# Kernel tuning notes

Hardware: AMD Instinct MI355X
Metric: run time of the kernel (lower is better)

Reference implementation:

```python
import jax, jax.numpy as jnp
import numpy as np

B, I, O = 512, 1024, 1024

def setup_inputs() -> dict:
    key = jax.random.key(0)
    kx, kw = jax.random.split(key)
    x = jax.random.normal(kx, (B, I), dtype=jnp.float32)
    W = jax.random.normal(kw, (O, I), dtype=jnp.float32)
    return {"x": x, "W": W}

def reference(x, W):
    # Tropical (max-plus) linear map: y[b, o] = max_i (x[b, i] + W[o, i])
    # Faithful to the torch broadcast-add + max-reduce formulation.
    out = x[..., None, :] + W[None, :, :]  # [B, O, I]
    return jnp.max(out, axis=-1)           # [B, O]
```

## Files before the change

kernel.cpp:

```cpp
#include <hip/hip_runtime.h>
#include <float.h>


#define B_DIM 512
#define I_DIM 1024
#define O_DIM 1024
#define BT 128
#define OT 128
#define KT 8

__device__ __forceinline__ void g2lds16(const float* g, float* l) {
    __builtin_amdgcn_global_load_lds(
        (const __attribute__((address_space(1))) void*)g,
        (__attribute__((address_space(3))) void*)l, 16, 0, 0);
}

__device__ __forceinline__ unsigned pack2h(float a, float b) {
    const unsigned lo = (unsigned)__builtin_bit_cast(unsigned short, (_Float16)a);
    const unsigned hi = (unsigned)__builtin_bit_cast(unsigned short, (_Float16)b);
    return lo | (hi << 16);
}
__device__ __forceinline__ float lo16f(unsigned u) {
    return (float)__builtin_bit_cast(_Float16, (unsigned short)(u & 0xffffu));
}
__device__ __forceinline__ float hi16f(unsigned u) {
    return (float)__builtin_bit_cast(_Float16, (unsigned short)(u >> 16));
}

template <int KB>
__global__ __launch_bounds__(256, 2) void trop_main(
    const float* __restrict__ xT,
    const float* __restrict__ wT,
    _Float16* __restrict__ part)
{
    constexpr int NCH = KB / KT;
    static_assert(KB % KT == 0, "");
    __shared__ __align__(16) float xs[4][2][KT * 32];
    __shared__ __align__(16) float ws[4][2][KT * 128];

    const int tid  = threadIdx.x;
    const int wave = tid >> 6;
    const int lane = tid & 63;
    const int to   = lane & 15;
    const int tbw  = lane >> 4;
    const int o0 = blockIdx.x * OT;
    const int b0 = blockIdx.y * BT;
    const int bw0 = b0 + 32 * wave;
    const int kz = blockIdx.z;
    const int kbase = kz * KB;

    const int rk8 = lane >> 3;
    const int xc4 = (lane & 7) * 4;
    const int rk2 = lane >> 5;
    const int wc4 = (lane & 31) * 4;

    float acc[8][8];
    #pragma unroll
    for (int i = 0; i < 8; ++i)
        #pragma unroll
        for (int j = 0; j < 8; ++j)
            acc[i][j] = -FLT_MAX;

    auto stage = [&](int c, int buf) {
        const int k0 = kbase + c * KT;
        g2lds16(&xT[(size_t)(k0 + rk8) * B_DIM + bw0 + xc4],
                &xs[wave][buf][0]);
        #pragma unroll
        for (int t = 0; t < 4; ++t)
            g2lds16(&wT[(size_t)(k0 + 2 * t + rk2) * O_DIM + o0 + wc4],
                    &ws[wave][buf][t * 256]);
    };

    auto compute = [&](int buf) {
        const float* xB = &xs[wave][buf][4 * tbw];
        const float* wB = &ws[wave][buf][4 * to];
        #pragma unroll
        for (int k = 0; k < KT; k += 2) {
            const float4 xa0 = *(const float4*)&xB[k * 32];
            const float4 xa1 = *(const float4*)&xB[k * 32 + 16];
            const float4 xb0 = *(const float4*)&xB[(k + 1) * 32];
            const float4 xb1 = *(const float4*)&xB[(k + 1) * 32 + 16];
            const float4 wa0 = *(const float4*)&wB[k * 128];
            const float4 wa1 = *(const float4*)&wB[k * 128 + 64];
            const float4 wb0 = *(const float4*)&wB[(k + 1) * 128];
            const float4 wb1 = *(const float4*)&wB[(k + 1) * 128 + 64];

            const float xa[8] = {xa0.x, xa0.y, xa0.z, xa0.w, xa1.x, xa1.y, xa1.z, xa1.w};
            const float xb[8] = {xb0.x, xb0.y, xb0.z, xb0.w, xb1.x, xb1.y, xb1.z, xb1.w};
            const float wa[8] = {wa0.x, wa0.y, wa0.z, wa0.w, wa1.x, wa1.y, wa1.z, wa1.w};
            const float wb[8] = {wb0.x, wb0.y, wb0.z, wb0.w, wb1.x, wb1.y, wb1.z, wb1.w};

            #pragma unroll
            for (int i = 0; i < 8; ++i)
                #pragma unroll
                for (int j = 0; j < 8; ++j) {
                    const float s0 = xa[i] + wa[j];
                    const float s1 = xb[i] + wb[j];
                    acc[i][j] = fmaxf(acc[i][j], fmaxf(s0, s1));
                }
        }
    };

    stage(0, 0);
    #pragma unroll
    for (int c = 0; c < NCH; ++c) {
        if (c + 1 < NCH) stage(c + 1, (c + 1) & 1);
        compute(c & 1);
    }

    _Float16* pout = part + (size_t)kz * (B_DIM * O_DIM);
    #pragma unroll
    for (int i = 0; i < 8; ++i) {
        const int b = bw0 + (i >> 2) * 16 + 4 * tbw + (i & 3);
        const uint2 v0 = make_uint2(pack2h(acc[i][0], acc[i][1]),
                                    pack2h(acc[i][2], acc[i][3]));
        const uint2 v1 = make_uint2(pack2h(acc[i][4], acc[i][5]),
                                    pack2h(acc[i][6], acc[i][7]));
        *(uint2*)((char*)pout + ((size_t)b * O_DIM + o0 + 4 * to) * 2)      = v0;
        *(uint2*)((char*)pout + ((size_t)b * O_DIM + o0 + 64 + 4 * to) * 2) = v1;
    }
}

__global__ __launch_bounds__(256) void transpose3(
    const float* __restrict__ x, float* __restrict__ xT,
    const float* __restrict__ W, float* __restrict__ wT)
{
    __shared__ float tile[32][33];
    const int tx = threadIdx.x;
    const int ty = threadIdx.y;
    const int z  = blockIdx.z;
    const float* in; float* out; int dst_ld;
    if (z == 0) { in = x;                  out = xT;            dst_ld = B_DIM; }
    else        { in = W + (size_t)(z - 1) * 512 * I_DIM;
                  out = wT + (z - 1) * 512;                     dst_ld = O_DIM; }
    const int r0 = blockIdx.y * 32;
    const int c0 = blockIdx.x * 32;
    #pragma unroll
    for (int i = 0; i < 4; ++i)
        tile[ty + 8 * i][tx] = in[(size_t)(r0 + ty + 8 * i) * I_DIM + c0 + tx];
    __syncthreads();
    #pragma unroll
    for (int i = 0; i < 4; ++i)
        out[(size_t)(c0 + ty + 8 * i) * dst_ld + r0 + tx] = tile[tx][ty + 8 * i];
}

template <int KS>
__global__ __launch_bounds__(256) void trop_reduce_h(
    const _Float16* __restrict__ part, float* __restrict__ y)
{
    constexpr size_t N = (size_t)B_DIM * O_DIM;
    const int idx = blockIdx.x * 256 + threadIdx.x;
    float m0 = -FLT_MAX, m1 = -FLT_MAX, m2 = -FLT_MAX, m3 = -FLT_MAX;
    float m4 = -FLT_MAX, m5 = -FLT_MAX, m6 = -FLT_MAX, m7 = -FLT_MAX;
    #pragma unroll
    for (int s = 0; s < KS; ++s) {
        const uint4 v = *(const uint4*)((const char*)part + (s * N + (size_t)idx * 8) * 2);
        m0 = fmaxf(m0, lo16f(v.x)); m1 = fmaxf(m1, hi16f(v.x));
        m2 = fmaxf(m2, lo16f(v.y)); m3 = fmaxf(m3, hi16f(v.y));
        m4 = fmaxf(m4, lo16f(v.z)); m5 = fmaxf(m5, hi16f(v.z));
        m6 = fmaxf(m6, lo16f(v.w)); m7 = fmaxf(m7, hi16f(v.w));
    }
    const float4 o0 = make_float4(m0, m1, m2, m3);
    const float4 o1 = make_float4(m4, m5, m6, m7);
    ((float4*)y)[2 * idx]     = o0;
    ((float4*)y)[2 * idx + 1] = o1;
}

__global__ __launch_bounds__(256) void trop_naive(
    const float* __restrict__ x, const float* __restrict__ W,
    float* __restrict__ y)
{
    const int idx = blockIdx.x * 256 + threadIdx.x;
    const int b = idx / O_DIM, o = idx % O_DIM;
    float m = -FLT_MAX;
    for (int i = 0; i < I_DIM; ++i)
        m = fmaxf(m, x[b * I_DIM + i] + W[o * I_DIM + i]);
    y[idx] = m;
}

extern "C" void kernel_launch(void* const* d_in, const int* in_sizes, int n_in,
                              void* d_out, int out_size, void* d_ws, size_t ws_size,
                              hipStream_t stream) {
    const float* x = (const float*)d_in[0];
    const float* W = (const float*)d_in[1];
    float* y = (float*)d_out;

    const size_t slab_h = (size_t)B_DIM * O_DIM * 2;
    const size_t xT_sz  = (size_t)B_DIM * I_DIM * sizeof(float);
    const size_t wT_sz  = (size_t)O_DIM * I_DIM * sizeof(float);
    const dim3 rgrid(B_DIM * O_DIM / 8 / 256);
    const dim3 tgrid(I_DIM / 32, 512 / 32, 3);
    const dim3 tblk(32, 8);

    if (ws_size >= 16 * slab_h + xT_sz + wT_sz) {
        _Float16* part = (_Float16*)d_ws;
        float* xT = (float*)((char*)d_ws + 16 * slab_h);
        float* wT = xT + (size_t)B_DIM * I_DIM;
        transpose3<<<tgrid, tblk, 0, stream>>>(x, xT, W, wT);
        trop_main<I_DIM / 16><<<dim3(O_DIM / OT, B_DIM / BT, 16), 256, 0, stream>>>(xT, wT, part);
        trop_reduce_h<16><<<rgrid, 256, 0, stream>>>(part, y);
    } else if (ws_size >= 8 * slab_h + xT_sz + wT_sz) {
        _Float16* part = (_Float16*)d_ws;
        float* xT = (float*)((char*)d_ws + 8 * slab_h);
        float* wT = xT + (size_t)B_DIM * I_DIM;
        transpose3<<<tgrid, tblk, 0, stream>>>(x, xT, W, wT);
        trop_main<I_DIM / 8><<<dim3(O_DIM / OT, B_DIM / BT, 8), 256, 0, stream>>>(xT, wT, part);
        trop_reduce_h<8><<<rgrid, 256, 0, stream>>>(part, y);
    } else if (ws_size >= slab_h + xT_sz + wT_sz) {
        _Float16* part = (_Float16*)d_ws;
        float* xT = (float*)((char*)d_ws + slab_h);
        float* wT = xT + (size_t)B_DIM * I_DIM;
        transpose3<<<tgrid, tblk, 0, stream>>>(x, xT, W, wT);
        trop_main<I_DIM><<<dim3(O_DIM / OT, B_DIM / BT, 1), 256, 0, stream>>>(xT, wT, part);
        trop_reduce_h<1><<<rgrid, 256, 0, stream>>>(part, y);
    } else {
        trop_naive<<<dim3(B_DIM * O_DIM / 256), 256, 0, stream>>>(x, W, y);
    }
}
```

Before: 86.94 us.

## Compute tropical max-plus in packed fp16 with v_pk_add/v_pk_max

Converts x and W to fp16 in the prep kernel: x keeps its row layout and W is transposed. The main kernel then runs the add and max on packed half2 values through inline v_pk_add_f16 and v_pk_max_f16, which halves the VALU instruction count per element pair. LDS staging and global loads move half as many bytes, and the x tile layout changes so each lane reads contiguous k values along with a new output store pattern. The cost is that the additions are now done in fp16 rather than fp32, which adds rounding error beyond the existing fp16 partial storage.

```diff
diff --git a/kernel.cpp b/kernel.cpp
--- a/kernel.cpp
+++ b/kernel.cpp
@@ -5,21 +5,32 @@
 #define B_DIM 512
 #define I_DIM 1024
 #define O_DIM 1024
-#define BT 128
-#define OT 128
-#define KT 8
-
-__device__ __forceinline__ void g2lds16(const float* g, float* l) {
+#define KT 16
+
+__device__ __forceinline__ void g2lds16(const void* g, void* l) {
     __builtin_amdgcn_global_load_lds(
         (const __attribute__((address_space(1))) void*)g,
         (__attribute__((address_space(3))) void*)l, 16, 0, 0);
 }
 
-__device__ __forceinline__ unsigned pack2h(float a, float b) {
-    const unsigned lo = (unsigned)__builtin_bit_cast(unsigned short, (_Float16)a);
-    const unsigned hi = (unsigned)__builtin_bit_cast(unsigned short, (_Float16)b);
-    return lo | (hi << 16);
-}
+__device__ __forceinline__ unsigned pk_add_bl(unsigned w, unsigned x) {
+    unsigned d;
+    asm("v_pk_add_f16 %0, %1, %2 op_sel:[0,0] op_sel_hi:[1,0]"
+        : "=v"(d) : "v"(w), "v"(x));
+    return d;
+}
+__device__ __forceinline__ unsigned pk_add_bh(unsigned w, unsigned x) {
+    unsigned d;
+    asm("v_pk_add_f16 %0, %1, %2 op_sel:[0,1] op_sel_hi:[1,1]"
+        : "=v"(d) : "v"(w), "v"(x));
+    return d;
+}
+__device__ __forceinline__ unsigned pk_max(unsigned a, unsigned b) {
+    unsigned d;
+    asm("v_pk_max_f16 %0, %1, %2" : "=v"(d) : "v"(a), "v"(b));
+    return d;
+}
+
 __device__ __forceinline__ float lo16f(unsigned u) {
     return (float)__builtin_bit_cast(_Float16, (unsigned short)(u & 0xffffu));
 }
@@ -29,75 +40,77 @@
 
 template <int KB>
 __global__ __launch_bounds__(256, 2) void trop_main(
-    const float* __restrict__ xT,
-    const float* __restrict__ wT,
+    const _Float16* __restrict__ xh,
+    const _Float16* __restrict__ wh,
     _Float16* __restrict__ part)
 {
     constexpr int NCH = KB / KT;
     static_assert(KB % KT == 0, "");
-    __shared__ __align__(16) float xs[4][2][KT * 32];
-    __shared__ __align__(16) float ws[4][2][KT * 128];
+    __shared__ __align__(16) char xs[4][2][32 * KT * 2];
+    __shared__ __align__(16) char ws[4][2][KT * 128 * 2];
 
     const int tid  = threadIdx.x;
     const int wave = tid >> 6;
     const int lane = tid & 63;
     const int to   = lane & 15;
     const int tbw  = lane >> 4;
-    const int o0 = blockIdx.x * OT;
-    const int b0 = blockIdx.y * BT;
-    const int bw0 = b0 + 32 * wave;
-    const int kz = blockIdx.z;
+    const int o0  = blockIdx.x * 128;
+    const int bw0 = blockIdx.y * 128 + 32 * wave;
+    const int kz  = blockIdx.z;
     const int kbase = kz * KB;
 
-    const int rk8 = lane >> 3;
-    const int xc4 = (lane & 7) * 4;
-    const int rk2 = lane >> 5;
-    const int wc4 = (lane & 31) * 4;
-
-    float acc[8][8];
+    const int xb_l = lane >> 1;
+    const int xk_l = (lane & 1) * 16;
+    const int wk_l = lane >> 4;
+    const int wc_l = (lane & 15) * 16;
+
+    unsigned acc_u[8][4];
     #pragma unroll
     for (int i = 0; i < 8; ++i)
         #pragma unroll
-        for (int j = 0; j < 8; ++j)
-            acc[i][j] = -FLT_MAX;
+        for (int p = 0; p < 4; ++p)
+            acc_u[i][p] = 0xFC00FC00u;
 
     auto stage = [&](int c, int buf) {
         const int k0 = kbase + c * KT;
-        g2lds16(&xT[(size_t)(k0 + rk8) * B_DIM + bw0 + xc4],
+        g2lds16((const char*)xh + ((size_t)(bw0 + xb_l) * I_DIM + k0) * 2 + xk_l,
                 &xs[wave][buf][0]);
         #pragma unroll
         for (int t = 0; t < 4; ++t)
-            g2lds16(&wT[(size_t)(k0 + 2 * t + rk2) * O_DIM + o0 + wc4],
-                    &ws[wave][buf][t * 256]);
+            g2lds16((const char*)wh + ((size_t)(k0 + 4 * t + wk_l) * O_DIM + o0) * 2 + wc_l,
+                    &ws[wave][buf][t * 1024]);
     };
 
     auto compute = [&](int buf) {
-        const float* xB = &xs[wave][buf][4 * tbw];
-        const float* wB = &ws[wave][buf][4 * to];
-        #pragma unroll
-        for (int k = 0; k < KT; k += 2) {
-            const float4 xa0 = *(const float4*)&xB[k * 32];
-            const float4 xa1 = *(const float4*)&xB[k * 32 + 16];
-            const float4 xb0 = *(const float4*)&xB[(k + 1) * 32];
-            const float4 xb1 = *(const float4*)&xB[(k + 1) * 32 + 16];
-            const float4 wa0 = *(const float4*)&wB[k * 128];
-            const float4 wa1 = *(const float4*)&wB[k * 128 + 64];
-            const float4 wb0 = *(const float4*)&wB[(k + 1) * 128];
-            const float4 wb1 = *(const float4*)&wB[(k + 1) * 128 + 64];
-
-            const float xa[8] = {xa0.x, xa0.y, xa0.z, xa0.w, xa1.x, xa1.y, xa1.z, xa1.w};
-            const float xb[8] = {xb0.x, xb0.y, xb0.z, xb0.w, xb1.x, xb1.y, xb1.z, xb1.w};
-            const float wa[8] = {wa0.x, wa0.y, wa0.z, wa0.w, wa1.x, wa1.y, wa1.z, wa1.w};
-            const float wb[8] = {wb0.x, wb0.y, wb0.z, wb0.w, wb1.x, wb1.y, wb1.z, wb1.w};
-
+        const char* xB = &xs[wave][buf][tbw * 32];
+        const char* wB = &ws[wave][buf][to * 16];
+        #pragma unroll
+        for (int h = 0; h < 2; ++h) {
+            unsigned xu[8][4];
             #pragma unroll
-            for (int i = 0; i < 8; ++i)
+            for (int i = 0; i < 8; ++i) {
+                const uint4 v = *(const uint4*)(xB + i * 128 + 16 * h);
+                xu[i][0] = v.x; xu[i][1] = v.y; xu[i][2] = v.z; xu[i][3] = v.w;
+            }
+            #pragma unroll
+            for (int q = 0; q < 4; ++q) {
+                const int k = 8 * h + 2 * q;
+                const uint4 w0 = *(const uint4*)(wB + k * 256);
+                const uint4 w1 = *(const uint4*)(wB + (k + 1) * 256);
                 #pragma unroll
-                for (int j = 0; j < 8; ++j) {
-                    const float s0 = xa[i] + wa[j];
-                    const float s1 = xb[i] + wb[j];
-                    acc[i][j] = fmaxf(acc[i][j], fmaxf(s0, s1));
+                for (int i = 0; i < 8; ++i) {
+                    const unsigned xp = xu[i][q];
+                    unsigned s0, s1;
+                    s0 = pk_add_bl(w0.x, xp); s1 = pk_add_bh(w1.x, xp);
+                    acc_u[i][0] = pk_max(acc_u[i][0], pk_max(s0, s1));
+                    s0 = pk_add_bl(w0.y, xp); s1 = pk_add_bh(w1.y, xp);
+                    acc_u[i][1] = pk_max(acc_u[i][1], pk_max(s0, s1));
+                    s0 = pk_add_bl(w0.z, xp); s1 = pk_add_bh(w1.z, xp);
+                    acc_u[i][2] = pk_max(acc_u[i][2], pk_max(s0, s1));
+                    s0 = pk_add_bl(w0.w, xp); s1 = pk_add_bh(w1.w, xp);
+                    acc_u[i][3] = pk_max(acc_u[i][3], pk_max(s0, s1));
                 }
+            }
         }
     };
 
@@ -111,37 +124,41 @@
     _Float16* pout = part + (size_t)kz * (B_DIM * O_DIM);
     #pragma unroll
     for (int i = 0; i < 8; ++i) {
-        const int b = bw0 + (i >> 2) * 16 + 4 * tbw + (i & 3);
-        const uint2 v0 = make_uint2(pack2h(acc[i][0], acc[i][1]),
-                                    pack2h(acc[i][2], acc[i][3]));
-        const uint2 v1 = make_uint2(pack2h(acc[i][4], acc[i][5]),
-                                    pack2h(acc[i][6], acc[i][7]));
-        *(uint2*)((char*)pout + ((size_t)b * O_DIM + o0 + 4 * to) * 2)      = v0;
-        *(uint2*)((char*)pout + ((size_t)b * O_DIM + o0 + 64 + 4 * to) * 2) = v1;
-    }
-}
-
-__global__ __launch_bounds__(256) void transpose3(
-    const float* __restrict__ x, float* __restrict__ xT,
-    const float* __restrict__ W, float* __restrict__ wT)
-{
-    __shared__ float tile[32][33];
+        const int b = bw0 + 4 * i + tbw;
+        const uint4 v = make_uint4(acc_u[i][0], acc_u[i][1],
+                                   acc_u[i][2], acc_u[i][3]);
+        *(uint4*)((char*)pout + ((size_t)b * O_DIM + o0 + 8 * to) * 2) = v;
+    }
+}
+
+__global__ __launch_bounds__(256) void prep_xw(
+    const float* __restrict__ x, _Float16* __restrict__ xh,
+    const float* __restrict__ W, _Float16* __restrict__ wh)
+{
     const int tx = threadIdx.x;
     const int ty = threadIdx.y;
     const int z  = blockIdx.z;
-    const float* in; float* out; int dst_ld;
-    if (z == 0) { in = x;                  out = xT;            dst_ld = B_DIM; }
-    else        { in = W + (size_t)(z - 1) * 512 * I_DIM;
-                  out = wT + (z - 1) * 512;                     dst_ld = O_DIM; }
     const int r0 = blockIdx.y * 32;
     const int c0 = blockIdx.x * 32;
+    if (z == 0) {
+        #pragma unroll
+        for (int i = 0; i < 4; ++i) {
+            const size_t idx = (size_t)(r0 + ty + 8 * i) * I_DIM + c0 + tx;
+            xh[idx] = (_Float16)x[idx];
+        }
+        return;
+    }
+    __shared__ float tile[32][33];
+    const float* in = W + (size_t)(z - 1) * 512 * I_DIM;
+    _Float16* out = wh + (z - 1) * 512;
     #pragma unroll
     for (int i = 0; i < 4; ++i)
         tile[ty + 8 * i][tx] = in[(size_t)(r0 + ty + 8 * i) * I_DIM + c0 + tx];
     __syncthreads();
     #pragma unroll
     for (int i = 0; i < 4; ++i)
-        out[(size_t)(c0 + ty + 8 * i) * dst_ld + r0 + tx] = tile[tx][ty + 8 * i];
+        out[(size_t)(c0 + ty + 8 * i) * O_DIM + r0 + tx] =
+            (_Float16)tile[tx][ty + 8 * i];
 }
 
 template <int KS>
@@ -186,32 +203,32 @@
     float* y = (float*)d_out;
 
     const size_t slab_h = (size_t)B_DIM * O_DIM * 2;
-    const size_t xT_sz  = (size_t)B_DIM * I_DIM * sizeof(float);
-    const size_t wT_sz  = (size_t)O_DIM * I_DIM * sizeof(float);
+    const size_t xh_sz  = (size_t)B_DIM * I_DIM * 2;
+    const size_t wh_sz  = (size_t)O_DIM * I_DIM * 2;
     const dim3 rgrid(B_DIM * O_DIM / 8 / 256);
     const dim3 tgrid(I_DIM / 32, 512 / 32, 3);
     const dim3 tblk(32, 8);
 
-    if (ws_size >= 16 * slab_h + xT_sz + wT_sz) {
+    if (ws_size >= 16 * slab_h + xh_sz + wh_sz) {
         _Float16* part = (_Float16*)d_ws;
-        float* xT = (float*)((char*)d_ws + 16 * slab_h);
-        float* wT = xT + (size_t)B_DIM * I_DIM;
-        transpose3<<<tgrid, tblk, 0, stream>>>(x, xT, W, wT);
-        trop_main<I_DIM / 16><<<dim3(O_DIM / OT, B_DIM / BT, 16), 256, 0, stream>>>(xT, wT, part);
+        _Float16* xh = (_Float16*)((char*)d_ws + 16 * slab_h);
+        _Float16* wh = xh + (size_t)B_DIM * I_DIM;
+        prep_xw<<<tgrid, tblk, 0, stream>>>(x, xh, W, wh);
+        trop_main<I_DIM / 16><<<dim3(8, 4, 16), 256, 0, stream>>>(xh, wh, part);
         trop_reduce_h<16><<<rgrid, 256, 0, stream>>>(part, y);
-    } else if (ws_size >= 8 * slab_h + xT_sz + wT_sz) {
+    } else if (ws_size >= 8 * slab_h + xh_sz + wh_sz) {
         _Float16* part = (_Float16*)d_ws;
-        float* xT = (float*)((char*)d_ws + 8 * slab_h);
-        float* wT = xT + (size_t)B_DIM * I_DIM;
-        transpose3<<<tgrid, tblk, 0, stream>>>(x, xT, W, wT);
-        trop_main<I_DIM / 8><<<dim3(O_DIM / OT, B_DIM / BT, 8), 256, 0, stream>>>(xT, wT, part);
+        _Float16* xh = (_Float16*)((char*)d_ws + 8 * slab_h);
+        _Float16* wh = xh + (size_t)B_DIM * I_DIM;
+        prep_xw<<<tgrid, tblk, 0, stream>>>(x, xh, W, wh);
+        trop_main<I_DIM / 8><<<dim3(8, 4, 8), 256, 0, stream>>>(xh, wh, part);
         trop_reduce_h<8><<<rgrid, 256, 0, stream>>>(part, y);
-    } else if (ws_size >= slab_h + xT_sz + wT_sz) {
+    } else if (ws_size >= slab_h + xh_sz + wh_sz) {
         _Float16* part = (_Float16*)d_ws;
-        float* xT = (float*)((char*)d_ws + slab_h);
-        float* wT = xT + (size_t)B_DIM * I_DIM;
-        transpose3<<<tgrid, tblk, 0, stream>>>(x, xT, W, wT);
-        trop_main<I_DIM><<<dim3(O_DIM / OT, B_DIM / BT, 1), 256, 0, stream>>>(xT, wT, part);
+        _Float16* xh = (_Float16*)((char*)d_ws + slab_h);
+        _Float16* wh = xh + (size_t)B_DIM * I_DIM;
+        prep_xw<<<tgrid, tblk, 0, stream>>>(x, xh, W, wh);
+        trop_main<I_DIM><<<dim3(8, 4, 1), 256, 0, stream>>>(xh, wh, part);
         trop_reduce_h<1><<<rgrid, 256, 0, stream>>>(part, y);
     } else {
         trop_naive<<<dim3(B_DIM * O_DIM / 256), 256, 0, stream>>>(x, W, y);
```

New measurement: 89.31 us. 1.03x slower.
